# Performance work log

Hardware: AMD Instinct MI355X
Metric: run time of the kernel (lower is better)

The kernel has to match this reference:

```python
import jax, jax.numpy as jnp
import numpy as np

C, H, W = 3, 224, 224
P = 14  # patches per row
PS = H // P  # 16
PATCH_DIM = C * PS * PS  # 768
HIDDEN = 768


def patchify(images):
    # images: [n, c, h, w] -> [n, P*P, c*PS*PS], flatten order (c, ph, pw)
    n = images.shape[0]
    x = images.reshape(n, C, P, PS, P, PS)
    x = x.transpose(0, 2, 4, 1, 3, 5)  # [n, Pi, Pj, c, ps, ps]
    return x.reshape(n, P * P, PATCH_DIM)


def setup_inputs() -> dict:
    key = jax.random.key(0)
    k1, k2, k3 = jax.random.split(key, 3)
    images = jax.random.normal(k1, (128, C, H, W), dtype=jnp.float32)
    # nn.Linear(patch_embedding_dim, hidden_dim): weight [out, in], bias [out]
    bound = 1.0 / np.sqrt(PATCH_DIM)
    W_lin = jax.random.uniform(k2, (HIDDEN, PATCH_DIM), minval=-bound, maxval=bound, dtype=jnp.float32)
    b_lin = jax.random.uniform(k3, (HIDDEN,), minval=-bound, maxval=bound, dtype=jnp.float32)
    cls_token = jnp.ones((1, HIDDEN), dtype=jnp.float32)
    return {"images": images, "W_lin": W_lin, "b_lin": b_lin, "cls_token": cls_token}


def reference(images, W_lin, b_lin, cls_token):
    patches = patchify(images)                        # [n, 196, 768]
    hidden = jnp.einsum('npd,hd->nph', patches, W_lin) + b_lin  # [n, 196, H]
    n = images.shape[0]
    cls = jnp.broadcast_to(cls_token[None], (n, 1, HIDDEN))
    return jnp.concatenate([cls, hidden], axis=1)     # [n, 197, H]
```

## Files before the change

kernel.cpp:

```cpp
#include <hip/hip_runtime.h>
#include <cstdint>


#define PGRID 14
#define PSZ   16
#define CHN   3
#define IMGW  224
#define KDIM  768
#define NDIM  768
#define NPATCH 196

typedef short bf16x8 __attribute__((ext_vector_type(8)));
typedef float f32x4  __attribute__((ext_vector_type(4)));

__device__ __forceinline__ short bf16rne(float f) {
    uint32_t u = __builtin_bit_cast(uint32_t, f);
    u += 0x7FFFu + ((u >> 16) & 1u);
    return (short)(u >> 16);
}

#define LDSTR 40

__global__ __launch_bounds__(256) void vit_gemm(
    const float* __restrict__ img, const float* __restrict__ Wl,
    const float* __restrict__ bias, float* __restrict__ out, int n_img)
{
    const int M = n_img * NPATCH;
    __shared__ short As[128 * LDSTR];
    __shared__ short Bs[128 * LDSTR];

    const int tid = threadIdx.x;
    const int m0 = blockIdx.y * 128;
    const int n0 = blockIdx.x * 128;

    const int col4  = tid & 7;
    const int rbase = tid >> 3;

    long arow[4];
    for (int rr = 0; rr < 4; ++rr) {
        int m = m0 + rbase + rr * 32;
        int mm = (m < M) ? m : (M - 1);
        int im = mm / NPATCH;
        int p  = mm % NPATCH;
        int Pi = p / PGRID;
        int Pj = p % PGRID;
        arow[rr] = ((long)(im * CHN) * IMGW + Pi * PSZ) * IMGW + Pj * PSZ;
    }

    const int lane = tid & 63;
    const int wave = tid >> 6;
    const int wm = (wave & 1) * 64;
    const int wn = (wave >> 1) * 64;
    const int wq = lane >> 4;
    const int lr = lane & 15;

    f32x4 acc[4][4] = {};

    for (int k0 = 0; k0 < KDIM; k0 += 32) {
        {
            int k  = k0 + col4 * 4;
            int c  = k >> 8;
            int ph = (k >> 4) & 15;
            int pw = k & 15;
            long koff = (long)(c * IMGW + ph) * IMGW + pw;
            #pragma unroll
            for (int rr = 0; rr < 4; ++rr) {
                const float4 v = *(const float4*)(img + arow[rr] + koff);
                int row = rbase + rr * 32;
                short4 s;
                s.x = bf16rne(v.x); s.y = bf16rne(v.y);
                s.z = bf16rne(v.z); s.w = bf16rne(v.w);
                *(short4*)(&As[row * LDSTR + col4 * 4]) = s;
            }
        }
        {
            int k = k0 + col4 * 4;
            #pragma unroll
            for (int rr = 0; rr < 4; ++rr) {
                int nrow = rbase + rr * 32;
                const float4 v = *(const float4*)(Wl + (long)(n0 + nrow) * KDIM + k);
                short4 s;
                s.x = bf16rne(v.x); s.y = bf16rne(v.y);
                s.z = bf16rne(v.z); s.w = bf16rne(v.w);
                *(short4*)(&Bs[nrow * LDSTR + col4 * 4]) = s;
            }
        }
        __syncthreads();

        bf16x8 a[4], b[4];
        #pragma unroll
        for (int i = 0; i < 4; ++i)
            a[i] = *(const bf16x8*)(&As[(wm + i * 16 + lr) * LDSTR + wq * 8]);
        #pragma unroll
        for (int i = 0; i < 4; ++i)
            b[i] = *(const bf16x8*)(&Bs[(wn + i * 16 + lr) * LDSTR + wq * 8]);
        #pragma unroll
        for (int i = 0; i < 4; ++i)
            #pragma unroll
            for (int j = 0; j < 4; ++j)
                acc[i][j] = __builtin_amdgcn_mfma_f32_16x16x32_bf16(a[i], b[j], acc[i][j], 0, 0, 0);
        __syncthreads();
    }

    float bv[4];
    #pragma unroll
    for (int j = 0; j < 4; ++j) bv[j] = bias[n0 + wn + j * 16 + lr];

    #pragma unroll
    for (int i = 0; i < 4; ++i) {
        #pragma unroll
        for (int r = 0; r < 4; ++r) {
            int gm = m0 + wm + i * 16 + wq * 4 + r;
            if (gm < M) {
                int im = gm / NPATCH;
                int p  = gm % NPATCH;
                long orow = ((long)im * 197 + 1 + p) * (long)NDIM;
                #pragma unroll
                for (int j = 0; j < 4; ++j) {
                    out[orow + n0 + wn + j * 16 + lr] = acc[i][j][r] + bv[j];
                }
            }
        }
    }
}

__global__ __launch_bounds__(256) void cls_fill(
    const float* __restrict__ cls, float* __restrict__ out, int n_img)
{
    int i = blockIdx.x * 256 + threadIdx.x;
    if (i < n_img * NDIM) {
        int im = i / NDIM;
        int n  = i - im * NDIM;
        out[(long)im * 197 * NDIM + n] = cls[n];
    }
}

extern "C" void kernel_launch(void* const* d_in, const int* in_sizes, int n_in,
                              void* d_out, int out_size, void* d_ws, size_t ws_size,
                              hipStream_t stream) {
    const float* img  = (const float*)d_in[0];
    const float* Wl   = (const float*)d_in[1];
    const float* bias = (const float*)d_in[2];
    const float* cls  = (const float*)d_in[3];
    float* out = (float*)d_out;

    int n_img = in_sizes[0] / (CHN * IMGW * IMGW);
    int M = n_img * NPATCH;

    dim3 grid(NDIM / 128, (M + 127) / 128);
    vit_gemm<<<grid, 256, 0, stream>>>(img, Wl, bias, out, n_img);

    int cls_elems = n_img * NDIM;
    cls_fill<<<(cls_elems + 255) / 256, 256, 0, stream>>>(cls, out, n_img);
}
```

Baseline: 201.2 us.

## Pre-convert patches and weights to bf16 workspace, GEMM via direct global-to-LDS loads

Adds pre-pass kernels that patchify the images and convert them, together with the weights, to bf16 in a workspace buffer. The cls fill is folded into the weight-conversion kernel. The GEMM then streams bf16 tiles with global_load_lds into XOR-swizzled LDS, using a K-step of 64 instead of 32, which removes per-tile conversion and strided image gathers from the main loop. This costs two extra kernel launches and an extra round trip of the bf16 activation matrix through memory. If the workspace is too small, the code falls back to the old kernel.

After: 193.9 us. 1.04x faster.

```diff
diff --git a/kernel.cpp b/kernel.cpp
--- a/kernel.cpp
+++ b/kernel.cpp
@@ -11,6 +11,7 @@
 #define NPATCH 196
 
 typedef short bf16x8 __attribute__((ext_vector_type(8)));
+typedef short short8v __attribute__((ext_vector_type(8)));
 typedef float f32x4  __attribute__((ext_vector_type(4)));
 
 __device__ __forceinline__ short bf16rne(float f) {
@@ -19,23 +20,155 @@
     return (short)(u >> 16);
 }
 
+__device__ __forceinline__ short8v cvt8(float4 v0, float4 v1) {
+    short8v s;
+    s[0] = bf16rne(v0.x); s[1] = bf16rne(v0.y); s[2] = bf16rne(v0.z); s[3] = bf16rne(v0.w);
+    s[4] = bf16rne(v1.x); s[5] = bf16rne(v1.y); s[6] = bf16rne(v1.z); s[7] = bf16rne(v1.w);
+    return s;
+}
+
+__device__ __forceinline__ void gload_lds16(const void* g, void* l) {
+    __builtin_amdgcn_global_load_lds(
+        (const __attribute__((address_space(1))) unsigned int*)g,
+        (__attribute__((address_space(3))) unsigned int*)l, 16, 0, 0);
+}
+
+__global__ __launch_bounds__(256) void prep_patch(
+    const float* __restrict__ img, short* __restrict__ A, int M)
+{
+    int t = blockIdx.x * 256 + threadIdx.x;
+    if (t >= M * 96) return;
+    int m  = t / 96;
+    int k8 = t - m * 96;
+    int k  = k8 * 8;
+    int c  = k >> 8;
+    int ph = (k >> 4) & 15;
+    int pw = k & 15;
+    int im = m / NPATCH;
+    int p  = m - im * NPATCH;
+    int Pi = p / PGRID;
+    int Pj = p - Pi * PGRID;
+    const float* src = img + (((long)(im * CHN + c) * IMGW + Pi * PSZ + ph) * IMGW + Pj * PSZ + pw);
+    float4 v0 = *(const float4*)src;
+    float4 v1 = *(const float4*)(src + 4);
+    *(short8v*)(A + (long)m * KDIM + k) = cvt8(v0, v1);
+}
+
+__global__ __launch_bounds__(256) void prep_small(
+    const float* __restrict__ Wl, const float* __restrict__ cls,
+    short* __restrict__ Wb, float* __restrict__ out, int n_img)
+{
+    int t = blockIdx.x * 256 + threadIdx.x;
+    const int WCH = KDIM * NDIM / 8;
+    if (t < WCH) {
+        float4 v0 = *(const float4*)(Wl + (long)t * 8);
+        float4 v1 = *(const float4*)(Wl + (long)t * 8 + 4);
+        *(short8v*)(Wb + (long)t * 8) = cvt8(v0, v1);
+    } else {
+        int u = t - WCH;
+        if (u < n_img * 96) {
+            int im = u / 96;
+            int k8 = u - im * 96;
+            float4 v0 = *(const float4*)(cls + k8 * 8);
+            float4 v1 = *(const float4*)(cls + k8 * 8 + 4);
+            float* dst = out + (long)im * 197 * NDIM + k8 * 8;
+            *(float4*)dst = v0;
+            *(float4*)(dst + 4) = v1;
+        }
+    }
+}
+
+__global__ __launch_bounds__(256) void vit_gemm2(
+    const short* __restrict__ A, const short* __restrict__ B,
+    const float* __restrict__ bias, float* __restrict__ out, int M)
+{
+    __shared__ short As[128 * 64];
+    __shared__ short Bs[128 * 64];
+
+    const int tid = threadIdx.x;
+    const int m0 = blockIdx.y * 128;
+    const int n0 = blockIdx.x * 128;
+    const int wave = tid >> 6;
+    const int lane = tid & 63;
+
+    const int srow = tid >> 3;
+    const int sk   = (tid & 7) ^ (srow & 7);
+    const long abase = (long)(m0 + srow) * KDIM + sk * 8;
+    const long bbase = (long)(n0 + srow) * KDIM + sk * 8;
+    char* AsB = (char*)As;
+    char* BsB = (char*)Bs;
+    const int ldsw = wave * 1024;
+
+    const int wm = (wave & 1) * 64;
+    const int wn = (wave >> 1) * 64;
+    const int wq = lane >> 4;
+    const int lr = lane & 15;
+    const int blk0 = ((wq)     ^ (lr & 7)) * 8;
+    const int blk1 = ((wq + 4) ^ (lr & 7)) * 8;
+
+    f32x4 acc[4][4] = {};
+
+    for (int kk = 0; kk < KDIM; kk += 64) {
+        #pragma unroll
+        for (int j = 0; j < 4; ++j) {
+            gload_lds16(A + abase + (long)j * 32 * KDIM + kk, AsB + j * 4096 + ldsw);
+            gload_lds16(B + bbase + (long)j * 32 * KDIM + kk, BsB + j * 4096 + ldsw);
+        }
+        __syncthreads();
+
+        #pragma unroll
+        for (int ks = 0; ks < 2; ++ks) {
+            const int blk = ks ? blk1 : blk0;
+            bf16x8 a[4], b[4];
+            #pragma unroll
+            for (int i = 0; i < 4; ++i)
+                a[i] = *(const bf16x8*)(&As[(wm + i * 16 + lr) * 64 + blk]);
+            #pragma unroll
+            for (int i = 0; i < 4; ++i)
+                b[i] = *(const bf16x8*)(&Bs[(wn + i * 16 + lr) * 64 + blk]);
+            #pragma unroll
+            for (int i = 0; i < 4; ++i)
+                #pragma unroll
+                for (int j = 0; j < 4; ++j)
+                    acc[i][j] = __builtin_amdgcn_mfma_f32_16x16x32_bf16(a[i], b[j], acc[i][j], 0, 0, 0);
+        }
+        __syncthreads();
+    }
+
+    float bv[4];
+    #pragma unroll
+    for (int j = 0; j < 4; ++j) bv[j] = bias[n0 + wn + j * 16 + lr];
+
+    #pragma unroll
+    for (int i = 0; i < 4; ++i) {
+        #pragma unroll
+        for (int r = 0; r < 4; ++r) {
+            int gm = m0 + wm + i * 16 + wq * 4 + r;
+            if (gm < M) {
+                int im = gm / NPATCH;
+                int p  = gm - im * NPATCH;
+                long orow = ((long)im * 197 + 1 + p) * (long)NDIM;
+                #pragma unroll
+                for (int j = 0; j < 4; ++j)
+                    out[orow + n0 + wn + j * 16 + lr] = acc[i][j][r] + bv[j];
+            }
+        }
+    }
+}
+
 #define LDSTR 40
-
-__global__ __launch_bounds__(256) void vit_gemm(
+__global__ __launch_bounds__(256) void vit_gemm_fb(
     const float* __restrict__ img, const float* __restrict__ Wl,
     const float* __restrict__ bias, float* __restrict__ out, int n_img)
 {
     const int M = n_img * NPATCH;
     __shared__ short As[128 * LDSTR];
     __shared__ short Bs[128 * LDSTR];
-
     const int tid = threadIdx.x;
     const int m0 = blockIdx.y * 128;
     const int n0 = blockIdx.x * 128;
-
     const int col4  = tid & 7;
     const int rbase = tid >> 3;
-
     long arow[4];
     for (int rr = 0; rr < 4; ++rr) {
         int m = m0 + rbase + rr * 32;
@@ -46,16 +179,13 @@
         int Pj = p % PGRID;
         arow[rr] = ((long)(im * CHN) * IMGW + Pi * PSZ) * IMGW + Pj * PSZ;
     }
-
     const int lane = tid & 63;
     const int wave = tid >> 6;
     const int wm = (wave & 1) * 64;
     const int wn = (wave >> 1) * 64;
     const int wq = lane >> 4;
     const int lr = lane & 15;
-
     f32x4 acc[4][4] = {};
-
     for (int k0 = 0; k0 < KDIM; k0 += 32) {
         {
             int k  = k0 + col4 * 4;
@@ -86,7 +216,6 @@
             }
         }
         __syncthreads();
-
         bf16x8 a[4], b[4];
         #pragma unroll
         for (int i = 0; i < 4; ++i)
@@ -101,11 +230,9 @@
                 acc[i][j] = __builtin_amdgcn_mfma_f32_16x16x32_bf16(a[i], b[j], acc[i][j], 0, 0, 0);
         __syncthreads();
     }
-
     float bv[4];
     #pragma unroll
     for (int j = 0; j < 4; ++j) bv[j] = bias[n0 + wn + j * 16 + lr];
-
     #pragma unroll
     for (int i = 0; i < 4; ++i) {
         #pragma unroll
@@ -116,9 +243,8 @@
                 int p  = gm % NPATCH;
                 long orow = ((long)im * 197 + 1 + p) * (long)NDIM;
                 #pragma unroll
-                for (int j = 0; j < 4; ++j) {
+                for (int j = 0; j < 4; ++j)
                     out[orow + n0 + wn + j * 16 + lr] = acc[i][j][r] + bv[j];
-                }
             }
         }
     }
@@ -146,10 +272,24 @@
 
     int n_img = in_sizes[0] / (CHN * IMGW * IMGW);
     int M = n_img * NPATCH;
-
-    dim3 grid(NDIM / 128, (M + 127) / 128);
-    vit_gemm<<<grid, 256, 0, stream>>>(img, Wl, bias, out, n_img);
-
-    int cls_elems = n_img * NDIM;
-    cls_fill<<<(cls_elems + 255) / 256, 256, 0, stream>>>(cls, out, n_img);
-}
+    int mblocks = (M + 127) / 128;
+    long Mpad = (long)mblocks * 128;
+
+    size_t need = (size_t)(Mpad * KDIM + (long)KDIM * NDIM) * sizeof(short);
+    if (ws_size >= need) {
+        short* A_ws = (short*)d_ws;
+        short* Wb   = A_ws + Mpad * KDIM;
+
+        prep_patch<<<(M * 96 + 255) / 256, 256, 0, stream>>>(img, A_ws, M);
+        int small_total = KDIM * NDIM / 8 + n_img * 96;
+        prep_small<<<(small_total + 255) / 256, 256, 0, stream>>>(Wl, cls, Wb, out, n_img);
+
+        dim3 grid(NDIM / 128, mblocks);
+        vit_gemm2<<<grid, 256, 0, stream>>>(A_ws, Wb, bias, out, M);
+    } else {
+        dim3 grid(NDIM / 128, mblocks);
+        vit_gemm_fb<<<grid, 256, 0, stream>>>(img, Wl, bias, out, n_img);
+        int cls_elems = n_img * NDIM;
+        cls_fill<<<(cls_elems + 255) / 256, 256, 0, stream>>>(cls, out, n_img);
+    }
+}
```
